# Optimization experiments

Measured on AMD Instinct MI355X. Metric: run time of the kernel, lower is better.

The kernel has to match this reference:

```python
import jax, jax.numpy as jnp
import numpy as np

N = 100000
E = 1600000
IN_C = 128
HID = 32
HEADS = 4
NUM_CLASSES = 16
NEG_SLOPE = 0.2


def setup_inputs() -> dict:
    key = jax.random.key(0)
    ks = jax.random.split(key, 10)
    x = jax.random.normal(ks[0], (N, IN_C), dtype=jnp.float32)
    edge_index = jax.random.randint(ks[1], (2, E), 0, N, dtype=jnp.int32)
    s1 = 1.0 / np.sqrt(IN_C)
    s2 = 1.0 / np.sqrt(HID * HEADS)
    W1 = jax.random.normal(ks[2], (IN_C, HEADS * HID), dtype=jnp.float32) * s1
    att_src1 = jax.random.normal(ks[3], (HEADS, HID), dtype=jnp.float32) * s1
    att_dst1 = jax.random.normal(ks[4], (HEADS, HID), dtype=jnp.float32) * s1
    b1 = jnp.zeros((HEADS * HID,), dtype=jnp.float32)
    W2 = jax.random.normal(ks[5], (HEADS * HID, NUM_CLASSES), dtype=jnp.float32) * s2
    att_src2 = jax.random.normal(ks[6], (1, NUM_CLASSES), dtype=jnp.float32) * s2
    att_dst2 = jax.random.normal(ks[7], (1, NUM_CLASSES), dtype=jnp.float32) * s2
    b2 = jnp.zeros((NUM_CLASSES,), dtype=jnp.float32)
    return {"x": x, "edge_index": edge_index,
            "W1": W1, "att_src1": att_src1, "att_dst1": att_dst1, "b1": b1,
            "W2": W2, "att_src2": att_src2, "att_dst2": att_dst2, "b2": b2}


def _gat_conv(x, src, dst, W, att_src, att_dst, b):
    # PyG GATConv: shared linear for src/dst, additive attention, segment softmax over dst.
    n = x.shape[0]
    H, C = att_src.shape
    h = (x @ W).reshape(n, H, C)                       # [N, H, C]
    a_s = jnp.einsum('nhc,hc->nh', h, att_src)          # [N, H]
    a_d = jnp.einsum('nhc,hc->nh', h, att_dst)          # [N, H]
    e = a_s[src] + a_d[dst]                             # [E, H]
    e = jnp.where(e >= 0, e, NEG_SLOPE * e)             # leaky_relu(0.2)
    # numerically stable segment softmax over destination node groups
    e_max = jax.ops.segment_max(e, dst, num_segments=n)
    e_exp = jnp.exp(e - e_max[dst])
    denom = jax.ops.segment_sum(e_exp, dst, num_segments=n)
    alpha = e_exp / denom[dst]                          # [E, H]
    msg = h[src] * alpha[:, :, None]                    # [E, H, C]
    out = jax.ops.segment_sum(msg, dst, num_segments=n) # [N, H, C]
    return out.reshape(n, H * C) + b


def reference(x, edge_index, W1, att_src1, att_dst1, b1, W2, att_src2, att_dst2, b2):
    n = x.shape[0]
    # add_self_loops=True (PyG default), same augmented edge set for both layers
    loop = jnp.arange(n, dtype=edge_index.dtype)
    src = jnp.concatenate([edge_index[0], loop])
    dst = jnp.concatenate([edge_index[1], loop])
    h = _gat_conv(x, src, dst, W1, att_src1, att_dst1, b1)
    h = jax.nn.elu(h)
    out = _gat_conv(h, src, dst, W2, att_src2, att_dst2, b2)
    return out
```

## Files before the change

### kernel.cpp

```cpp
#include <hip/hip_runtime.h>
#include <hip/hip_bf16.h>
#include <math.h>


typedef unsigned short u16;
typedef unsigned int u32;
typedef __attribute__((ext_vector_type(8))) short bf16x8;
typedef __attribute__((ext_vector_type(4))) float f32x4;

__device__ __forceinline__ float eluf(float v) { return v > 0.f ? v : expm1f(v); }
__device__ __forceinline__ u16 f2bf(float f) {
    u32 u = __float_as_uint(f);
    u += 0x7fff + ((u >> 16) & 1);
    return (u16)(u >> 16);
}
__device__ __forceinline__ float bf2f(u16 u) {
    return __uint_as_float(((u32)u) << 16);
}
__device__ __forceinline__ float expleaky(float e) {
    float m = e >= 0.f ? 1.44269504f : 0.28853901f;
    return exp2f(e * m);
}

__global__ __launch_bounds__(256) void ksetup(
    const float* __restrict__ W1, const float* __restrict__ W2,
    const float* __restrict__ ats2, const float* __restrict__ atd2,
    u16* __restrict__ w1fh, u16* __restrict__ w1fl,
    float* __restrict__ u, float* __restrict__ v, u16* __restrict__ w2tb,
    int* __restrict__ deg, int N)
{
    const int b = blockIdx.x, tid = threadIdx.x;
    if (b < 64) {
        int idx = b * 256 + tid;
        int j = idx & 7, l = (idx >> 3) & 63, q = (idx >> 9) & 3, ct = idx >> 11;
        int k = q * 32 + (l >> 4) * 8 + j;
        int n = ct * 16 + (l & 15);
        float w = W1[k * 128 + n];
        u16 hv = f2bf(w);
        w1fh[idx] = hv;
        w1fl[idx] = f2bf(w - bf2f(hv));
    } else if (b == 64) {
        if (tid < 128) {
            float su = 0.f, sv = 0.f;
            #pragma unroll
            for (int j = 0; j < 16; ++j) {
                float w = W2[tid * 16 + j];
                su = fmaf(w, ats2[j], su);
                sv = fmaf(w, atd2[j], sv);
                w2tb[j * 128 + tid] = f2bf(w);
            }
            u[tid] = su; v[tid] = sv;
        }
    } else {
        int z = (b - 65) * 1024 + tid * 4;
        if (z < N) *(int4*)&deg[z] = make_int4(0, 0, 0, 0);
    }
}

#define REPW 40
__global__ __launch_bounds__(256) void mega1(
    const float* __restrict__ x, const u16* __restrict__ w1fh,
    const u16* __restrict__ w1fl,
    const float* __restrict__ att_s, const float* __restrict__ att_d,
    u16* __restrict__ h1b, float* __restrict__ as1, float* __restrict__ ad1,
    int N,
    const int* __restrict__ ei, int* __restrict__ deg, int* __restrict__ rank,
    int E, int KB)
{
    __shared__ u16 rep[4][16 * REPW];
    const int tid = threadIdx.x;
    const int b = blockIdx.x;

    if (b % 3 == 0) {
        const int base = (b / 3) * 2048 + tid;
        int dd[8];
        #pragma unroll
        for (int k = 0; k < 8; ++k) {
            int e = base + 256 * k;
            dd[k] = (e < E) ? ei[E + e] : -1;
        }
        int rk[8];
        #pragma unroll
        for (int k = 0; k < 8; ++k)
            if (dd[k] >= 0) rk[k] = atomicAdd(&deg[dd[k]], 1);
        #pragma unroll
        for (int k = 0; k < 8; ++k) {
            int e = base + 256 * k;
            if (e < E) rank[e] = rk[k];
        }
        return;
    }

    const int g = b - b / 3 - 1;
    const int GB = 2 * KB;
    const int wv = tid >> 6, lane = tid & 63;
    const int m = lane & 15, quad = lane >> 4;
    const int h = wv;

    bf16x8 bh[2][4], bl[2][4];
    #pragma unroll
    for (int sub = 0; sub < 2; ++sub) {
        #pragma unroll
        for (int q = 0; q < 4; ++q) {
            const int off = (((2 * h + sub) * 4 + q) * 64 + lane) * 8;
            bh[sub][q] = *(const bf16x8*)&w1fh[off];
            bl[sub][q] = *(const bf16x8*)&w1fl[off];
        }
    }

    const float cs0 = att_s[h * 32 + m];
    const float cs1 = att_s[h * 32 + 16 + m];
    const float cd0 = att_d[h * 32 + m];
    const float cd1 = att_d[h * 32 + 16 + m];

    u16* myrep = rep[wv];
    const int ntile = (N + 15) >> 4;

    for (int t = g; t < ntile; t += GB) {
        const int r0 = t << 4;
        int arow = r0 + m;
        if (arow >= N) arow = N - 1;
        const float* xr = &x[(size_t)arow * 128 + quad * 8];

        bf16x8 ah[4], al[4];
        #pragma unroll
        for (int q = 0; q < 4; ++q) {
            float4 f0 = *(const float4*)&xr[q * 32];
            float4 f1 = *(const float4*)&xr[q * 32 + 4];
            float fv[8] = {f0.x, f0.y, f0.z, f0.w, f1.x, f1.y, f1.z, f1.w};
            union { u16 us[8]; bf16x8 v; } hh, lu;
            #pragma unroll
            for (int j = 0; j < 8; ++j) {
                u16 hvv = f2bf(fv[j]);
                hh.us[j] = hvv;
                lu.us[j] = f2bf(fv[j] - bf2f(hvv));
            }
            ah[q] = hh.v; al[q] = lu.v;
        }

        f32x4 acc[2];
        #pragma unroll
        for (int sub = 0; sub < 2; ++sub) {
            f32x4 a = {0.f, 0.f, 0.f, 0.f};
            #pragma unroll
            for (int q = 0; q < 4; ++q) {
                a = __builtin_amdgcn_mfma_f32_16x16x32_bf16(ah[q], bh[sub][q], a, 0, 0, 0);
                a = __builtin_amdgcn_mfma_f32_16x16x32_bf16(al[q], bh[sub][q], a, 0, 0, 0);
                a = __builtin_amdgcn_mfma_f32_16x16x32_bf16(ah[q], bl[sub][q], a, 0, 0, 0);
            }
            acc[sub] = a;
        }

        float sp[4], dp[4];
        #pragma unroll
        for (int r = 0; r < 4; ++r) {
            sp[r] = fmaf(acc[0][r], cs0, acc[1][r] * cs1);
            dp[r] = fmaf(acc[0][r], cd0, acc[1][r] * cd1);
        }
        #pragma unroll
        for (int r = 0; r < 4; ++r) {
            sp[r] += __shfl_xor(sp[r], 1); sp[r] += __shfl_xor(sp[r], 2);
            sp[r] += __shfl_xor(sp[r], 4); sp[r] += __shfl_xor(sp[r], 8);
            dp[r] += __shfl_xor(dp[r], 1); dp[r] += __shfl_xor(dp[r], 2);
            dp[r] += __shfl_xor(dp[r], 4); dp[r] += __shfl_xor(dp[r], 8);
        }
        if (m == 0) {
            #pragma unroll
            for (int r = 0; r < 4; ++r) {
                int rr = r0 + quad * 4 + r;
                if (rr < N) {
                    as1[rr * 4 + h] = sp[r];
                    ad1[rr * 4 + h] = dp[r];
                }
            }
        }

        #pragma unroll
        for (int sub = 0; sub < 2; ++sub) {
            #pragma unroll
            for (int r = 0; r < 4; ++r)
                myrep[(quad * 4 + r) * REPW + sub * 16 + m] = f2bf(acc[sub][r]);
        }
        __asm__ __volatile__("s_waitcnt lgkmcnt(0)" ::: "memory");
        __builtin_amdgcn_sched_barrier(0);
        const int rr = lane >> 2, cc = lane & 3;
        uint4 vv = *(const uint4*)&myrep[rr * REPW + cc * 8];
        const int grow = r0 + rr;
        if (grow < N)
            *(uint4*)&h1b[(size_t)grow * 128 + h * 32 + cc * 8] = vv;
    }
}

__global__ __launch_bounds__(256) void kscan1(
    const int* __restrict__ deg, int* __restrict__ rowptr,
    int* __restrict__ bsum, int N)
{
    __shared__ int lds[256];
    const int t = threadIdx.x;
    const int base = blockIdx.x * 1024 + t * 4;
    int v[4];
    int s = 0;
    #pragma unroll
    for (int j = 0; j < 4; ++j) {
        v[j] = (base + j < N) ? deg[base + j] : 0;
        s += v[j];
    }
    lds[t] = s;
    __syncthreads();
    for (int off = 1; off < 256; off <<= 1) {
        int y = (t >= off) ? lds[t - off] : 0;
        __syncthreads();
        lds[t] += y;
        __syncthreads();
    }
    int run = lds[t] - s;
    #pragma unroll
    for (int j = 0; j < 4; ++j) {
        if (base + j < N) rowptr[base + j] = run;
        run += v[j];
    }
    if (t == 255) bsum[blockIdx.x] = lds[255];
}

__global__ __launch_bounds__(128) void kscan2(int* __restrict__ bsum, int NB)
{
    __shared__ int lds[128];
    const int t = threadIdx.x;
    int v = (t < NB) ? bsum[t] : 0;
    lds[t] = v;
    __syncthreads();
    for (int off = 1; off < 128; off <<= 1) {
        int y = (t >= off) ? lds[t - off] : 0;
        __syncthreads();
        lds[t] += y;
        __syncthreads();
    }
    if (t < NB) bsum[t] = lds[t] - v;
}

__global__ __launch_bounds__(256) void kscat(
    const int* __restrict__ ei, const int* __restrict__ rowptr,
    const int* __restrict__ bsum, const int* __restrict__ rank,
    int* __restrict__ colidx, int E)
{
    int e = blockIdx.x * 256 + threadIdx.x;
    if (e >= E) return;
    int s = ei[e], d = ei[E + e];
    colidx[rowptr[d] + bsum[d >> 10] + rank[e]] = s;
}

__global__ __launch_bounds__(256) void kg1(
    const int* __restrict__ rowptr, const int* __restrict__ bsum,
    const int* __restrict__ colidx,
    const u16* __restrict__ h1b, const float* __restrict__ as1,
    const float* __restrict__ ad1, const float* __restrict__ b1,
    const float* __restrict__ u, const float* __restrict__ v,
    u16* __restrict__ x2b, float* __restrict__ as2, float* __restrict__ ad2,
    int N, int E)
{
    const int d = blockIdx.x * 4 + (threadIdx.x >> 6);
    if (d >= N) return;
    const int lane = threadIdx.x & 63;
    const int c = lane * 2;
    const int headB = lane >> 4;
    const int headA = lane & 3;
    const int eA = lane >> 2;

    const float adA = ad1[d * 4 + headA];
    const float wself = expleaky(as1[d * 4 + headB] + ad1[d * 4 + headB]);
    u32 hd = *(const u32*)&h1b[(d << 7) + c];
    float accx = wself * bf2f((u16)hd);
    float accy = wself * bf2f((u16)(hd >> 16));
    float den = wself;

    int i0r = rowptr[d] + bsum[d >> 10];
    int i1r = (d + 1 == N) ? E : rowptr[d + 1] + bsum[(d + 1) >> 10];
    const int i0 = __builtin_amdgcn_readfirstlane(i0r);
    const int i1 = __builtin_amdgcn_readfirstlane(i1r);

    for (int i = i0; i < i1; i += 16) {
        const int nb = min(16, i1 - i);
        const int ii = i + eA;
        const int iic = ii < i1 ? ii : i0;
        int sAv = colidx[iic];
        float wA = expleaky(as1[(sAv << 2) + headA] + adA);
        wA = (ii < i1) ? wA : 0.f;
        int e = 0;
        for (; e + 8 <= nb; e += 8) {
            int s0 = colidx[i + e + 0];
            int s1 = colidx[i + e + 1];
            int s2 = colidx[i + e + 2];
            int s3 = colidx[i + e + 3];
            int s4 = colidx[i + e + 4];
            int s5 = colidx[i + e + 5];
            int s6 = colidx[i + e + 6];
            int s7 = colidx[i + e + 7];
            float w0 = __shfl(wA, ((e + 0) << 2) + headB);
            float w1 = __shfl(wA, ((e + 1) << 2) + headB);
            float w2 = __shfl(wA, ((e + 2) << 2) + headB);
            float w3 = __shfl(wA, ((e + 3) << 2) + headB);
            float w4 = __shfl(wA, ((e + 4) << 2) + headB);
            float w5 = __shfl(wA, ((e + 5) << 2) + headB);
            float w6 = __shfl(wA, ((e + 6) << 2) + headB);
            float w7 = __shfl(wA, ((e + 7) << 2) + headB);
            u32 v0 = *(const u32*)&h1b[(s0 << 7) + c];
            u32 v1 = *(const u32*)&h1b[(s1 << 7) + c];
            u32 v2 = *(const u32*)&h1b[(s2 << 7) + c];
            u32 v3 = *(const u32*)&h1b[(s3 << 7) + c];
            u32 v4 = *(const u32*)&h1b[(s4 << 7) + c];
            u32 v5 = *(const u32*)&h1b[(s5 << 7) + c];
            u32 v6 = *(const u32*)&h1b[(s6 << 7) + c];
            u32 v7 = *(const u32*)&h1b[(s7 << 7) + c];
            accx = fmaf(w0, bf2f((u16)v0), accx); accy = fmaf(w0, bf2f((u16)(v0 >> 16)), accy);
            accx = fmaf(w1, bf2f((u16)v1), accx); accy = fmaf(w1, bf2f((u16)(v1 >> 16)), accy);
            accx = fmaf(w2, bf2f((u16)v2), accx); accy = fmaf(w2, bf2f((u16)(v2 >> 16)), accy);
            accx = fmaf(w3, bf2f((u16)v3), accx); accy = fmaf(w3, bf2f((u16)(v3 >> 16)), accy);
            accx = fmaf(w4, bf2f((u16)v4), accx); accy = fmaf(w4, bf2f((u16)(v4 >> 16)), accy);
            accx = fmaf(w5, bf2f((u16)v5), accx); accy = fmaf(w5, bf2f((u16)(v5 >> 16)), accy);
            accx = fmaf(w6, bf2f((u16)v6), accx); accy = fmaf(w6, bf2f((u16)(v6 >> 16)), accy);
            accx = fmaf(w7, bf2f((u16)v7), accx); accy = fmaf(w7, bf2f((u16)(v7 >> 16)), accy);
            den += ((w0 + w1) + (w2 + w3)) + ((w4 + w5) + (w6 + w7));
        }
        for (; e < nb; ++e) {
            int s = colidx[i + e];
            float w = __shfl(wA, (e << 2) + headB);
            u32 hv = *(const u32*)&h1b[(s << 7) + c];
            accx = fmaf(w, bf2f((u16)hv), accx);
            accy = fmaf(w, bf2f((u16)(hv >> 16)), accy);
            den += w;
        }
    }

    const float inv = 1.f / den;
    const float2 bv = *(const float2*)&b1[c];
    const float x2a = eluf(fmaf(accx, inv, bv.x));
    const float x2c = eluf(fmaf(accy, inv, bv.y));

    u32 pk = ((u32)f2bf(x2c) << 16) | (u32)f2bf(x2a);
    *(u32*)&x2b[(d << 7) + c] = pk;

    const float2 uv = *(const float2*)&u[c];
    const float2 vv = *(const float2*)&v[c];
    float sA = fmaf(x2a, uv.x, x2c * uv.y);
    float sB = fmaf(x2a, vv.x, x2c * vv.y);
    #pragma unroll
    for (int m = 1; m < 64; m <<= 1) {
        sA += __shfl_xor(sA, m);
        sB += __shfl_xor(sB, m);
    }
    if (lane == 0) { as2[d] = sA; ad2[d] = sB; }
}

__global__ __launch_bounds__(256) void kh2(
    const u16* __restrict__ x2b, const u16* __restrict__ w2tb,
    u16* __restrict__ h2b, int N)
{
    const int wv = threadIdx.x >> 6, lane = threadIdx.x & 63;
    const int n0 = blockIdx.x * 64 + wv * 16;
    if (n0 >= N) return;
    const int m = lane & 15;
    const int kq = lane >> 4;
    bf16x8 bfr[4];
    #pragma unroll
    for (int q = 0; q < 4; ++q)
        bfr[q] = *(const bf16x8*)&w2tb[m * 128 + q * 32 + kq * 8];

    int ar = n0 + m;
    if (ar >= N) ar = N - 1;
    const u16* arow = &x2b[((size_t)ar << 7) + kq * 8];
    f32x4 acc = {0.f, 0.f, 0.f, 0.f};
    #pragma unroll
    for (int q = 0; q < 4; ++q) {
        bf16x8 af = *(const bf16x8*)&arow[q * 32];
        acc = __builtin_amdgcn_mfma_f32_16x16x32_bf16(af, bfr[q], acc, 0, 0, 0);
    }
    #pragma unroll
    for (int r = 0; r < 4; ++r) {
        int rr = n0 + kq * 4 + r;
        if (rr < N) h2b[((size_t)rr << 4) + m] = f2bf(acc[r]);
    }
}

__global__ __launch_bounds__(256) void kg2(
    const int* __restrict__ rowptr, const int* __restrict__ bsum,
    const int* __restrict__ colidx,
    const u16* __restrict__ h2b, const float* __restrict__ as2,
    const float* __restrict__ ad2, const float* __restrict__ b2,
    float* __restrict__ out, int N, int E)
{
    const int d = blockIdx.x * 4 + (threadIdx.x >> 6);
    if (d >= N) return;
    const int lane = threadIdx.x & 63;
    const int ch = lane & 7, g = lane >> 3;

    const float ad_d = ad2[d];
    float acc0 = 0.f, acc1 = 0.f, den = 0.f;
    int i0r = rowptr[d] + bsum[d >> 10];
    int i1r = (d + 1 == N) ? E : rowptr[d + 1] + bsum[(d + 1) >> 10];
    const int i0 = __builtin_amdgcn_readfirstlane(i0r);
    const int i1 = __builtin_amdgcn_readfirstlane(i1r);

    for (int i = i0; i < i1; i += 64) {
        const int nb = min(64, i1 - i);
        const int idx = i + lane;
        const int idxc = idx < i1 ? idx : i0;
        int sA = colidx[idxc];
        float wA = expleaky(as2[sA] + ad_d);
        wA = (idx < i1) ? wA : 0.f;
        const int kU = (nb + 7) >> 3;
        for (int k = 0; k < kU; ++k) {
            int e = g + 8 * k;
            int ec = e < nb ? e : 0;
            float w = __shfl(wA, ec);
            int s = __shfl(sA, ec);
            if (e >= nb) w = 0.f;
            u32 hv = *(const u32*)&h2b[(s << 4) + ch * 2];
            acc0 = fmaf(w, bf2f((u16)hv), acc0);
            acc1 = fmaf(w, bf2f((u16)(hv >> 16)), acc1);
            den += w;
        }
    }
    acc0 += __shfl_xor(acc0, 8); acc0 += __shfl_xor(acc0, 16); acc0 += __shfl_xor(acc0, 32);
    acc1 += __shfl_xor(acc1, 8); acc1 += __shfl_xor(acc1, 16); acc1 += __shfl_xor(acc1, 32);
    den  += __shfl_xor(den, 8);  den  += __shfl_xor(den, 16);  den  += __shfl_xor(den, 32);

    const float wself = expleaky(as2[d] + ad_d);
    u32 hd = *(const u32*)&h2b[(d << 4) + ch * 2];
    acc0 = fmaf(wself, bf2f((u16)hd), acc0);
    acc1 = fmaf(wself, bf2f((u16)(hd >> 16)), acc1);
    den += wself;
    if (g == 0) {
        float2 ov = {acc0 / den + b2[ch * 2], acc1 / den + b2[ch * 2 + 1]};
        *(float2*)&out[(d << 4) + ch * 2] = ov;
    }
}

extern "C" void kernel_launch(void* const* d_in, const int* in_sizes, int n_in,
                              void* d_out, int out_size, void* d_ws, size_t ws_size,
                              hipStream_t stream) {
    const float* x    = (const float*)d_in[0];
    const int*   ei   = (const int*)d_in[1];
    const float* W1   = (const float*)d_in[2];
    const float* ats1 = (const float*)d_in[3];
    const float* atd1 = (const float*)d_in[4];
    const float* b1   = (const float*)d_in[5];
    const float* W2   = (const float*)d_in[6];
    const float* ats2 = (const float*)d_in[7];
    const float* atd2 = (const float*)d_in[8];
    const float* b2   = (const float*)d_in[9];
    float* out = (float*)d_out;
    const int N = in_sizes[0] / 128;
    const int E = in_sizes[1] / 2;

    u16* h1b   = (u16*)d_ws;
    u16* x2b   = h1b + (size_t)N * 128;
    u16* h2b   = x2b + (size_t)N * 128;
    u16* w2tb  = h2b + (size_t)N * 16;
    u16* w1fh  = w2tb + 2048;
    u16* w1fl  = w1fh + 16384;
    float* as1 = (float*)(w1fl + 16384);
    float* ad1 = as1 + (size_t)N * 4;
    float* as2 = ad1 + (size_t)N * 4;
    float* ad2 = as2 + N;
    float* u   = ad2 + N;
    float* v   = u + 128;
    int* deg    = (int*)(v + 128);
    int* rowptr = deg + ((N + 7) & ~3);
    int* bsum   = rowptr + ((N + 7) & ~3);
    int* colidx = bsum + 128;
    int* rank   = colidx + E;

    const int NB = (N + 1023) / 1024;
    const int KB = (E + 2047) / 2048;
    const int G1 = 3 * KB;

    hipLaunchKernelGGL(ksetup, dim3(65 + NB), dim3(256), 0, stream,
                       W1, W2, ats2, atd2, w1fh, w1fl, u, v, w2tb, deg, N);
    hipLaunchKernelGGL(mega1, dim3(G1), dim3(256), 0, stream,
                       x, w1fh, w1fl, ats1, atd1, h1b, as1, ad1, N,
                       ei, deg, rank, E, KB);
    hipLaunchKernelGGL(kscan1, dim3(NB), dim3(256), 0, stream,
                       deg, rowptr, bsum, N);
    hipLaunchKernelGGL(kscan2, dim3(1), dim3(128), 0, stream, bsum, NB);
    hipLaunchKernelGGL(kscat, dim3((E + 255) / 256), dim3(256), 0, stream,
                       ei, rowptr, bsum, rank, colidx, E);
    hipLaunchKernelGGL(kg1, dim3((N + 3) / 4), dim3(256), 0, stream,
                       rowptr, bsum, colidx, h1b, as1, ad1, b1, u, v,
                       x2b, as2, ad2, N, E);
    hipLaunchKernelGGL(kh2, dim3((N + 63) / 64), dim3(256), 0, stream,
                       x2b, w2tb, h2b, N);
    hipLaunchKernelGGL(kg2, dim3((N + 3) / 4), dim3(256), 0, stream,
                       rowptr, bsum, colidx, h2b, as2, ad2, b2, out, N, E);
}
```

Measured before the change: 348.0 us.

## Split layer-1 aggregation into two half-channel passes for cache locality

Layer-1 neighbour aggregation now runs as two launches, each gathering only 64 of the 128 bf16 channels (two heads) per node. Each pass touches half of the h1 feature table, so the randomly gathered working set is more likely to stay resident in cache. In exchange, the CSR indices and attention logits are read twice, each lane does 2-byte gathers instead of 4-byte ones, and there is an extra launch. The second pass accumulates into as2/ad2 with a read-modify-write that relies on the first pass having finished.

```diff
diff --git a/kernel.cpp b/kernel.cpp
--- a/kernel.cpp
+++ b/kernel.cpp
@@ -249,28 +249,28 @@
     colidx[rowptr[d] + bsum[d >> 10] + rank[e]] = s;
 }
 
-__global__ __launch_bounds__(256) void kg1(
+__global__ __launch_bounds__(256) void kg1h(
     const int* __restrict__ rowptr, const int* __restrict__ bsum,
     const int* __restrict__ colidx,
     const u16* __restrict__ h1b, const float* __restrict__ as1,
     const float* __restrict__ ad1, const float* __restrict__ b1,
     const float* __restrict__ u, const float* __restrict__ v,
     u16* __restrict__ x2b, float* __restrict__ as2, float* __restrict__ ad2,
-    int N, int E)
+    int N, int E, int coff)
 {
     const int d = blockIdx.x * 4 + (threadIdx.x >> 6);
     if (d >= N) return;
     const int lane = threadIdx.x & 63;
-    const int c = lane * 2;
-    const int headB = lane >> 4;
-    const int headA = lane & 3;
-    const int eA = lane >> 2;
+    const int hbase = coff >> 5;
+    const int hsel = lane >> 5;
+    const int hh = hbase + hsel;
+    const int headA = hbase + (lane & 1);
+    const int eA = lane >> 1;
+    const int c = coff + lane;
 
     const float adA = ad1[d * 4 + headA];
-    const float wself = expleaky(as1[d * 4 + headB] + ad1[d * 4 + headB]);
-    u32 hd = *(const u32*)&h1b[(d << 7) + c];
-    float accx = wself * bf2f((u16)hd);
-    float accy = wself * bf2f((u16)(hd >> 16));
+    const float wself = expleaky(as1[d * 4 + hh] + ad1[d * 4 + hh]);
+    float acc = wself * bf2f(h1b[(d << 7) + c]);
     float den = wself;
 
     int i0r = rowptr[d] + bsum[d >> 10];
@@ -278,8 +278,10 @@
     const int i0 = __builtin_amdgcn_readfirstlane(i0r);
     const int i1 = __builtin_amdgcn_readfirstlane(i1r);
 
-    for (int i = i0; i < i1; i += 16) {
-        const int nb = min(16, i1 - i);
+    const u16* hp = h1b + c;
+
+    for (int i = i0; i < i1; i += 32) {
+        const int nb = min(32, i1 - i);
         const int ii = i + eA;
         const int iic = ii < i1 ? ii : i0;
         int sAv = colidx[iic];
@@ -295,60 +297,56 @@
             int s5 = colidx[i + e + 5];
             int s6 = colidx[i + e + 6];
             int s7 = colidx[i + e + 7];
-            float w0 = __shfl(wA, ((e + 0) << 2) + headB);
-            float w1 = __shfl(wA, ((e + 1) << 2) + headB);
-            float w2 = __shfl(wA, ((e + 2) << 2) + headB);
-            float w3 = __shfl(wA, ((e + 3) << 2) + headB);
-            float w4 = __shfl(wA, ((e + 4) << 2) + headB);
-            float w5 = __shfl(wA, ((e + 5) << 2) + headB);
-            float w6 = __shfl(wA, ((e + 6) << 2) + headB);
-            float w7 = __shfl(wA, ((e + 7) << 2) + headB);
-            u32 v0 = *(const u32*)&h1b[(s0 << 7) + c];
-            u32 v1 = *(const u32*)&h1b[(s1 << 7) + c];
-            u32 v2 = *(const u32*)&h1b[(s2 << 7) + c];
-            u32 v3 = *(const u32*)&h1b[(s3 << 7) + c];
-            u32 v4 = *(const u32*)&h1b[(s4 << 7) + c];
-            u32 v5 = *(const u32*)&h1b[(s5 << 7) + c];
-            u32 v6 = *(const u32*)&h1b[(s6 << 7) + c];
-            u32 v7 = *(const u32*)&h1b[(s7 << 7) + c];
-            accx = fmaf(w0, bf2f((u16)v0), accx); accy = fmaf(w0, bf2f((u16)(v0 >> 16)), accy);
-            accx = fmaf(w1, bf2f((u16)v1), accx); accy = fmaf(w1, bf2f((u16)(v1 >> 16)), accy);
-            accx = fmaf(w2, bf2f((u16)v2), accx); accy = fmaf(w2, bf2f((u16)(v2 >> 16)), accy);
-            accx = fmaf(w3, bf2f((u16)v3), accx); accy = fmaf(w3, bf2f((u16)(v3 >> 16)), accy);
-            accx = fmaf(w4, bf2f((u16)v4), accx); accy = fmaf(w4, bf2f((u16)(v4 >> 16)), accy);
-            accx = fmaf(w5, bf2f((u16)v5), accx); accy = fmaf(w5, bf2f((u16)(v5 >> 16)), accy);
-            accx = fmaf(w6, bf2f((u16)v6), accx); accy = fmaf(w6, bf2f((u16)(v6 >> 16)), accy);
-            accx = fmaf(w7, bf2f((u16)v7), accx); accy = fmaf(w7, bf2f((u16)(v7 >> 16)), accy);
+            float w0 = __shfl(wA, ((e + 0) << 1) + hsel);
+            float w1 = __shfl(wA, ((e + 1) << 1) + hsel);
+            float w2 = __shfl(wA, ((e + 2) << 1) + hsel);
+            float w3 = __shfl(wA, ((e + 3) << 1) + hsel);
+            float w4 = __shfl(wA, ((e + 4) << 1) + hsel);
+            float w5 = __shfl(wA, ((e + 5) << 1) + hsel);
+            float w6 = __shfl(wA, ((e + 6) << 1) + hsel);
+            float w7 = __shfl(wA, ((e + 7) << 1) + hsel);
+            u16 v0 = hp[s0 << 7];
+            u16 v1 = hp[s1 << 7];
+            u16 v2 = hp[s2 << 7];
+            u16 v3 = hp[s3 << 7];
+            u16 v4 = hp[s4 << 7];
+            u16 v5 = hp[s5 << 7];
+            u16 v6 = hp[s6 << 7];
+            u16 v7 = hp[s7 << 7];
+            acc = fmaf(w0, bf2f(v0), acc);
+            acc = fmaf(w1, bf2f(v1), acc);
+            acc = fmaf(w2, bf2f(v2), acc);
+            acc = fmaf(w3, bf2f(v3), acc);
+            acc = fmaf(w4, bf2f(v4), acc);
+            acc = fmaf(w5, bf2f(v5), acc);
+            acc = fmaf(w6, bf2f(v6), acc);
+            acc = fmaf(w7, bf2f(v7), acc);
             den += ((w0 + w1) + (w2 + w3)) + ((w4 + w5) + (w6 + w7));
         }
         for (; e < nb; ++e) {
             int s = colidx[i + e];
-            float w = __shfl(wA, (e << 2) + headB);
-            u32 hv = *(const u32*)&h1b[(s << 7) + c];
-            accx = fmaf(w, bf2f((u16)hv), accx);
-            accy = fmaf(w, bf2f((u16)(hv >> 16)), accy);
+            float w = __shfl(wA, (e << 1) + hsel);
+            acc = fmaf(w, bf2f(hp[s << 7]), acc);
             den += w;
         }
     }
 
     const float inv = 1.f / den;
-    const float2 bv = *(const float2*)&b1[c];
-    const float x2a = eluf(fmaf(accx, inv, bv.x));
-    const float x2c = eluf(fmaf(accy, inv, bv.y));
-
-    u32 pk = ((u32)f2bf(x2c) << 16) | (u32)f2bf(x2a);
-    *(u32*)&x2b[(d << 7) + c] = pk;
-
-    const float2 uv = *(const float2*)&u[c];
-    const float2 vv = *(const float2*)&v[c];
-    float sA = fmaf(x2a, uv.x, x2c * uv.y);
-    float sB = fmaf(x2a, vv.x, x2c * vv.y);
+    const float x2v = eluf(fmaf(acc, inv, b1[c]));
+
+    x2b[(d << 7) + c] = f2bf(x2v);
+
+    float sA = x2v * u[c];
+    float sB = x2v * v[c];
     #pragma unroll
     for (int m = 1; m < 64; m <<= 1) {
         sA += __shfl_xor(sA, m);
         sB += __shfl_xor(sB, m);
     }
-    if (lane == 0) { as2[d] = sA; ad2[d] = sB; }
+    if (lane == 0) {
+        if (coff == 0) { as2[d] = sA; ad2[d] = sB; }
+        else { as2[d] += sA; ad2[d] += sB; }
+    }
 }
 
 __global__ __launch_bounds__(256) void kh2(
@@ -484,9 +482,12 @@
     hipLaunchKernelGGL(kscan2, dim3(1), dim3(128), 0, stream, bsum, NB);
     hipLaunchKernelGGL(kscat, dim3((E + 255) / 256), dim3(256), 0, stream,
                        ei, rowptr, bsum, rank, colidx, E);
-    hipLaunchKernelGGL(kg1, dim3((N + 3) / 4), dim3(256), 0, stream,
+    hipLaunchKernelGGL(kg1h, dim3((N + 3) / 4), dim3(256), 0, stream,
                        rowptr, bsum, colidx, h1b, as1, ad1, b1, u, v,
-                       x2b, as2, ad2, N, E);
+                       x2b, as2, ad2, N, E, 0);
+    hipLaunchKernelGGL(kg1h, dim3((N + 3) / 4), dim3(256), 0, stream,
+                       rowptr, bsum, colidx, h1b, as1, ad1, b1, u, v,
+                       x2b, as2, ad2, N, E, 64);
     hipLaunchKernelGGL(kh2, dim3((N + 63) / 64), dim3(256), 0, stream,
                        x2b, w2tb, h2b, N);
     hipLaunchKernelGGL(kg2, dim3((N + 3) / 4), dim3(256), 0, stream,
```

New measurement: 385.7 us. +10.8%, slower.

## Split fused histogram/GEMM kernel into separate launches with retuned grid

Applied to the files above, without the earlier changes.

Splits the combined kernel, which interleaved degree-histogram atomics with the layer-1 feature GEMM by block index, into two separate kernels. The GEMM kernel now runs with a grid of about a quarter of the row tiles, so each block handles roughly four tiles, and empty asm statements pin the preloaded weight fragments in registers. This removes the heterogeneous block mix and per-block branching but gives up the overlap of atomic-bound and compute-bound work within one launch. It also adds a kernel launch.

```diff
diff --git a/kernel.cpp b/kernel.cpp
--- a/kernel.cpp
+++ b/kernel.cpp
@@ -57,42 +57,38 @@
     }
 }
 
+__global__ __launch_bounds__(256) void khist(
+    const int* __restrict__ ei, int* __restrict__ deg, int* __restrict__ rank,
+    int E)
+{
+    const int base = blockIdx.x * 2048 + threadIdx.x;
+    int dd[8];
+    #pragma unroll
+    for (int k = 0; k < 8; ++k) {
+        int e = base + 256 * k;
+        dd[k] = (e < E) ? ei[E + e] : -1;
+    }
+    int rk[8];
+    #pragma unroll
+    for (int k = 0; k < 8; ++k)
+        if (dd[k] >= 0) rk[k] = atomicAdd(&deg[dd[k]], 1);
+    #pragma unroll
+    for (int k = 0; k < 8; ++k) {
+        int e = base + 256 * k;
+        if (e < E) rank[e] = rk[k];
+    }
+}
+
 #define REPW 40
-__global__ __launch_bounds__(256) void mega1(
+__global__ __launch_bounds__(256) void kgemm(
     const float* __restrict__ x, const u16* __restrict__ w1fh,
     const u16* __restrict__ w1fl,
     const float* __restrict__ att_s, const float* __restrict__ att_d,
     u16* __restrict__ h1b, float* __restrict__ as1, float* __restrict__ ad1,
-    int N,
-    const int* __restrict__ ei, int* __restrict__ deg, int* __restrict__ rank,
-    int E, int KB)
+    int N, int GB)
 {
     __shared__ u16 rep[4][16 * REPW];
     const int tid = threadIdx.x;
-    const int b = blockIdx.x;
-
-    if (b % 3 == 0) {
-        const int base = (b / 3) * 2048 + tid;
-        int dd[8];
-        #pragma unroll
-        for (int k = 0; k < 8; ++k) {
-            int e = base + 256 * k;
-            dd[k] = (e < E) ? ei[E + e] : -1;
-        }
-        int rk[8];
-        #pragma unroll
-        for (int k = 0; k < 8; ++k)
-            if (dd[k] >= 0) rk[k] = atomicAdd(&deg[dd[k]], 1);
-        #pragma unroll
-        for (int k = 0; k < 8; ++k) {
-            int e = base + 256 * k;
-            if (e < E) rank[e] = rk[k];
-        }
-        return;
-    }
-
-    const int g = b - b / 3 - 1;
-    const int GB = 2 * KB;
     const int wv = tid >> 6, lane = tid & 63;
     const int m = lane & 15, quad = lane >> 4;
     const int h = wv;
@@ -107,6 +103,14 @@
             bl[sub][q] = *(const bf16x8*)&w1fl[off];
         }
     }
+    #pragma unroll
+    for (int sub = 0; sub < 2; ++sub) {
+        #pragma unroll
+        for (int q = 0; q < 4; ++q) {
+            asm volatile("" : "+v"(bh[sub][q]));
+            asm volatile("" : "+v"(bl[sub][q]));
+        }
+    }
 
     const float cs0 = att_s[h * 32 + m];
     const float cs1 = att_s[h * 32 + 16 + m];
@@ -116,7 +120,7 @@
     u16* myrep = rep[wv];
     const int ntile = (N + 15) >> 4;
 
-    for (int t = g; t < ntile; t += GB) {
+    for (int t = blockIdx.x; t < ntile; t += GB) {
         const int r0 = t << 4;
         int arow = r0 + m;
         if (arow >= N) arow = N - 1;
@@ -472,13 +476,15 @@
 
     const int NB = (N + 1023) / 1024;
     const int KB = (E + 2047) / 2048;
-    const int G1 = 3 * KB;
+    const int ntile = (N + 15) / 16;
+    const int GB = (ntile + 3) / 4;
 
     hipLaunchKernelGGL(ksetup, dim3(65 + NB), dim3(256), 0, stream,
                        W1, W2, ats2, atd2, w1fh, w1fl, u, v, w2tb, deg, N);
-    hipLaunchKernelGGL(mega1, dim3(G1), dim3(256), 0, stream,
-                       x, w1fh, w1fl, ats1, atd1, h1b, as1, ad1, N,
-                       ei, deg, rank, E, KB);
+    hipLaunchKernelGGL(khist, dim3(KB), dim3(256), 0, stream,
+                       ei, deg, rank, E);
+    hipLaunchKernelGGL(kgemm, dim3(GB), dim3(256), 0, stream,
+                       x, w1fh, w1fl, ats1, atd1, h1b, as1, ad1, N, GB);
     hipLaunchKernelGGL(kscan1, dim3(NB), dim3(256), 0, stream,
                        deg, rowptr, bsum, N);
     hipLaunchKernelGGL(kscan2, dim3(1), dim3(128), 0, stream, bsum, NB);
```

Result: slower. 365.5 us (+5.0%).
